# Optimization experiments

Measured on AMD Instinct MI355X. Metric: run time of the kernel, lower is better.

The kernel has to match this reference:

```python
import jax, jax.numpy as jnp
from jax import lax
import numpy as np

B, S, T = 128, 256, 256
VOCAB, EMBED, ENC, DEC, DOF, LOOKBACK = 32000, 256, 256, 512, 4, 4


def setup_inputs() -> dict:
    key = jax.random.key(0)
    ks = jax.random.split(key, 20)
    w = lambda k, shape: jax.random.normal(k, shape, jnp.float32) * 0.05
    return {
        "in_seq": jax.random.randint(ks[0], (B, S), 0, VOCAB),
        "tgt_seq": jax.random.normal(ks[1], (B, T, DOF), jnp.float32),
        "lengths": jnp.full((B,), S, dtype=jnp.int32),
        "embedding": w(ks[2], (VOCAB, EMBED)),
        "enc_Wih_f": w(ks[3], (4 * ENC, EMBED)),
        "enc_Whh_f": w(ks[4], (4 * ENC, ENC)),
        "enc_b_f": w(ks[5], (4 * ENC,)),
        "enc_Wih_b": w(ks[6], (4 * ENC, EMBED)),
        "enc_Whh_b": w(ks[7], (4 * ENC, ENC)),
        "enc_b_b": w(ks[8], (4 * ENC,)),
        "dec_Wih": w(ks[9], (4 * DEC, DEC + LOOKBACK * DOF)),
        "dec_Whh": w(ks[10], (4 * DEC, DEC)),
        "dec_b": w(ks[11], (4 * DEC,)),
        "W_src": w(ks[12], (DEC, 2 * ENC)),
        "W_ctx": w(ks[13], (DEC, 2 * ENC + DEC)),
        "W_out": w(ks[14], (DOF, DEC)),
        "b_out": w(ks[15], (DOF,)),
    }


def _lstm_cell(x, h, c, Wih, Whh, b):
    # PyTorch gate order: i, f, g, o
    g = x @ Wih.T + h @ Whh.T + b
    i, f, gg, o = jnp.split(g, 4, axis=-1)
    c_new = jax.nn.sigmoid(f) * c + jax.nn.sigmoid(i) * jnp.tanh(gg)
    h_new = jax.nn.sigmoid(o) * jnp.tanh(c_new)
    return h_new, c_new


def _scan_lstm(xs, Wih, Whh, b, reverse=False):
    # xs: [T, B, E] -> hidden states [T, B, H] (aligned to original time order)
    Bsz, H = xs.shape[1], Whh.shape[1]
    h0 = jnp.zeros((Bsz, H), xs.dtype)

    def step(carry, x):
        h, c = carry
        h, c = _lstm_cell(x, h, c, Wih, Whh, b)
        return (h, c), h

    _, hs = lax.scan(step, (h0, h0), xs, reverse=reverse)
    return hs


def reference(in_seq, tgt_seq, lengths, embedding,
              enc_Wih_f, enc_Whh_f, enc_b_f,
              enc_Wih_b, enc_Whh_b, enc_b_b,
              dec_Wih, dec_Whh, dec_b,
              W_src, W_ctx, W_out, b_out):
    Bsz, Tlen = tgt_seq.shape[0], tgt_seq.shape[1]
    # ----- encoder (bi-LSTM, eval mode: dropout off, zero initial state) -----
    emb = embedding[in_seq]              # [B,S,E]
    xs = jnp.swapaxes(emb, 0, 1)         # [S,B,E]
    hf = _scan_lstm(xs, enc_Wih_f, enc_Whh_f, enc_b_f, reverse=False)
    hb = _scan_lstm(xs, enc_Wih_b, enc_Whh_b, enc_b_b, reverse=True)
    enc_out = jnp.swapaxes(jnp.concatenate([hf, hb], axis=-1), 0, 1)  # [B,S,2H]
    enc_mask = (in_seq == 0)             # [B,S]
    # precompute attention source projection once (same math as per-step)
    proj = jnp.einsum('bse,de->bsd', enc_out, W_src)  # [B,S,DEC]
    # ----- teacher-forced lookback windows of target frames -----
    pad = jnp.concatenate([jnp.zeros((Bsz, LOOKBACK, DOF), tgt_seq.dtype), tgt_seq], axis=1)
    win = jnp.stack([pad[:, k:k + Tlen] for k in range(LOOKBACK)], axis=2)  # [B,T,LB,DOF]
    win = win.reshape(Bsz, Tlen, LOOKBACK * DOF)
    win_t = jnp.swapaxes(win, 0, 1)      # [T,B,LB*DOF]
    h0 = jnp.zeros((Bsz, DEC), tgt_seq.dtype)

    def step(carry, w_t):
        h, c, feed = carry
        x = jnp.concatenate([w_t, feed], axis=-1)         # [B, LB*DOF + DEC]
        h, c = _lstm_cell(x, h, c, dec_Wih, dec_Whh, dec_b)
        scores = jnp.einsum('bd,bsd->bs', h, proj)        # Luong general score
        scores = jnp.where(enc_mask, -jnp.inf, scores)
        aw = jax.nn.softmax(scores, axis=-1)              # [B,S]
        ctx = jnp.einsum('bs,bse->be', aw, enc_out)       # [B,2H]
        feed = jnp.tanh(jnp.concatenate([h, ctx], axis=-1) @ W_ctx.T)
        out = feed @ W_out.T + b_out                      # [B,DOF]
        return (h, c, feed), (out, aw)

    _, (outs, aws) = lax.scan(step, (h0, h0, h0), win_t)
    dec_outputs = jnp.swapaxes(outs, 0, 1)   # [B,T,DOF]
    attn_weights = jnp.swapaxes(aws, 0, 1)   # [B,T,S]
    outputs = jnp.concatenate(
        [jnp.tanh(dec_outputs[..., :-1]), jax.nn.relu(dec_outputs[..., -1:])], axis=-1)
    return outputs, attn_weights
```

## Files before the change

### kernel.cpp

```cpp
#include <hip/hip_runtime.h>
#include <stdint.h>

#define B 128
#define S 256
#define T 256
#define EMBED 256
#define ENC 256
#define DEC 512
#define DOF 4

typedef __attribute__((ext_vector_type(8))) short bf16x8;
typedef __attribute__((ext_vector_type(4))) float f32x4;

static __device__ __forceinline__ float bf2f(unsigned short u){
  union{uint32_t u;float f;}c; c.u = ((uint32_t)u)<<16; return c.f;
}
static __device__ __forceinline__ unsigned short f2bf(float f){
  union{float f;uint32_t u;}c; c.f=f; uint32_t u=c.u;
  u += 0x7fffu + ((u>>16)&1u);
  return (unsigned short)(u>>16);
}
static __device__ __forceinline__ void unp2(uint32_t w, float&a, float&b){
  union{uint32_t u;float f;}c1,c2; c1.u = w<<16; c2.u = w & 0xffff0000u; a=c1.f; b=c2.f;
}
static __device__ __forceinline__ float sigm(float x){ return 1.0f/(1.0f+__expf(-x)); }

static __device__ __forceinline__ unsigned long long ldc8(const void* p){
  return __hip_atomic_load((unsigned long long*)p, __ATOMIC_RELAXED, __HIP_MEMORY_SCOPE_AGENT);
}
static __device__ __forceinline__ void stc8(void* p, unsigned long long v){
  __hip_atomic_store((unsigned long long*)p, v, __ATOMIC_RELAXED, __HIP_MEMORY_SCOPE_AGENT);
}
static __device__ __forceinline__ void stc4(void* p, unsigned v){
  __hip_atomic_store((unsigned*)p, v, __ATOMIC_RELAXED, __HIP_MEMORY_SCOPE_AGENT);
}
static __device__ __forceinline__ void stc4f(float* p, float v){
  __hip_atomic_store((unsigned*)p, __float_as_uint(v), __ATOMIC_RELAXED, __HIP_MEMORY_SCOPE_AGENT);
}
static __device__ __forceinline__ float ldc4f(const float* p){
  return __uint_as_float(__hip_atomic_load((const unsigned*)p, __ATOMIC_RELAXED, __HIP_MEMORY_SCOPE_AGENT));
}
union F16x8 { unsigned long long q[2]; bf16x8 v; unsigned short s[8]; };
union Ubf   { bf16x8 v; uint32_t u[4]; unsigned short s[8]; };
static __device__ __forceinline__ bf16x8 ldfrag_c(const unsigned short* p){
  F16x8 u; u.q[0] = ldc8(p); u.q[1] = ldc8(p + 4); return u.v;
}
static __device__ __forceinline__ unsigned long long pack4bf(float a,float b,float c,float d){
  return (unsigned long long)f2bf(a) | ((unsigned long long)f2bf(b)<<16)
       | ((unsigned long long)f2bf(c)<<32) | ((unsigned long long)f2bf(d)<<48);
}

#define CLINE 32
#define A_OFF 0
#define F_OFF 128
#define PAIR_OFF 192
#define ENC_OFF 320
static __device__ __forceinline__ unsigned* cl(unsigned* c, int line){ return c + (size_t)line*CLINE; }

static __device__ __forceinline__ void bar_arr(unsigned* line){
  __builtin_amdgcn_s_waitcnt(0);
  __syncthreads();
  if (threadIdx.x == 0)
    __hip_atomic_fetch_add(line, 1u, __ATOMIC_RELAXED, __HIP_MEMORY_SCOPE_AGENT);
}
static __device__ __forceinline__ void barw(unsigned* set, unsigned target, int mask){
  if (threadIdx.x < 64){
    unsigned* p = set + (size_t)(threadIdx.x & mask)*CLINE;
    const int mine = (int)threadIdx.x <= mask;
    for (;;){
      int ok = 1;
      if (mine)
        ok = (int)(__hip_atomic_load(p, __ATOMIC_RELAXED, __HIP_MEMORY_SCOPE_AGENT) >= target);
      if (__all(ok)) break;
      __builtin_amdgcn_s_sleep(8);
    }
  }
  __syncthreads();
  asm volatile("" ::: "memory");
}

static __device__ __forceinline__ int enc_idx(int s, int c){
  return s*256 + (((c & 24) | ((c ^ s) & 7)) << 3);
}

__global__ __launch_bounds__(256,1) void k_encoder(
  const unsigned short* __restrict__ emb,
  const unsigned short* __restrict__ WF, const unsigned short* __restrict__ WB,
  const float* __restrict__ bF, const float* __restrict__ bB,
  unsigned short* __restrict__ hEnc,
  unsigned short* __restrict__ encOut,
  unsigned* __restrict__ cntBase)
{
  __shared__ __align__(16) unsigned short Ws[16*520];
  __shared__ __align__(16) float Gs[64*17];
  __shared__ float bsh[16];
  const int bid = blockIdx.x;
  const int dir = bid >> 7;
  const int mg  = (bid >> 6) & 1;
  const int ng  = bid & 63;
  const int tid = threadIdx.x;
  const int lane = tid & 63, w = tid >> 6;
  const int l16 = lane & 15, qd = lane >> 4;
  const int m_base = mg * 64;
  unsigned* mycnt = cntBase + (size_t)dir*16*CLINE;
  unsigned* myline = cl(mycnt, bid & 15);

  const unsigned short* Wg = (dir ? WB : WF) + (size_t)ng*16*512;
  for (int i = tid; i < 16*64; i += 256){
    const int r = i >> 6, s = i & 63;
    *(uint4*)&Ws[r*520 + s*8] = *(const uint4*)&Wg[r*512 + s*8];
  }
  if (tid < 16) bsh[tid] = (dir ? bB : bF)[ng*16 + tid];
  float c[4] = {0.f,0.f,0.f,0.f};
  __syncthreads();

  for (int t = 0; t < S; ++t){
    const int tt = dir ? (S-1-t) : t;
    const unsigned short* Ae = emb + ((size_t)tt*B + m_base + w*16 + l16)*256 + qd*8;
    bf16x8 av[8];
#pragma unroll
    for (int ks = 0; ks < 8; ++ks) av[ks] = *(const bf16x8*)(Ae + ks*32);
    if (t) barw(mycnt, (unsigned)(8u*(unsigned)t), 15);
    const unsigned short* Ah = hEnc + (((size_t)dir*2 + (size_t)(t&1))*B + m_base + w*16 + l16)*256 + qd*8;
    bf16x8 hf[8];
#pragma unroll
    for (int ks = 0; ks < 8; ++ks) hf[ks] = ldfrag_c(Ah + ks*32);
    f32x4 acc = (f32x4){0.f,0.f,0.f,0.f};
#pragma unroll
    for (int ks = 0; ks < 8; ++ks){
      bf16x8 bb = *(const bf16x8*)&Ws[l16*520 + ks*32 + qd*8];
      acc = __builtin_amdgcn_mfma_f32_16x16x32_bf16(av[ks], bb, acc, 0, 0, 0);
    }
#pragma unroll
    for (int ks = 0; ks < 8; ++ks){
      bf16x8 bb = *(const bf16x8*)&Ws[l16*520 + 256 + ks*32 + qd*8];
      acc = __builtin_amdgcn_mfma_f32_16x16x32_bf16(hf[ks], bb, acc, 0, 0, 0);
    }
    __syncthreads();
#pragma unroll
    for (int r = 0; r < 4; ++r)
      Gs[(w*16 + qd*4 + r)*17 + l16] = acc[r];
    __syncthreads();
    if (tid < 64){
      const int bl = tid;
      float hv[4];
#pragma unroll
      for (int u = 0; u < 4; ++u){
        const float gi = Gs[bl*17 + u*4 + 0] + bsh[u*4 + 0];
        const float gf = Gs[bl*17 + u*4 + 1] + bsh[u*4 + 1];
        const float gg = Gs[bl*17 + u*4 + 2] + bsh[u*4 + 2];
        const float go = Gs[bl*17 + u*4 + 3] + bsh[u*4 + 3];
        const float cn = sigm(gf)*c[u] + sigm(gi)*tanhf(gg);
        c[u] = cn;
        hv[u] = sigm(go)*tanhf(cn);
      }
      const int b2 = m_base + bl;
      const unsigned long long hq = pack4bf(hv[0],hv[1],hv[2],hv[3]);
      stc8(&hEnc[(((size_t)dir*2 + (size_t)((t+1)&1))*B + b2)*256 + ng*4], hq);
      *(unsigned long long*)&encOut[((size_t)b2*S + tt)*512 + dir*256 + ng*4] = hq;
    }
    bar_arr(myline);
  }
}

__global__ __launch_bounds__(256,2) void k_proj(
  const unsigned short* __restrict__ encOut,
  const unsigned short* __restrict__ WSP,
  const unsigned short* __restrict__ WCP,
  unsigned short* __restrict__ proj,
  unsigned short* __restrict__ encW)
{
  const int nb = blockIdx.x & 7;
  const int mt = blockIdx.x >> 3;
  const int tid = threadIdx.x;
  const int lane = tid & 63, w = tid >> 6;
  const int l16 = lane & 15, qd = lane >> 4;
  const int m0 = mt*64 + w*16;
  const unsigned short* Ap = encOut + ((size_t)m0 + l16)*512 + qd*8;
  bf16x8 av[16];
#pragma unroll
  for (int ks = 0; ks < 16; ++ks) av[ks] = *(const bf16x8*)(Ap + ks*32);
  for (int which = 0; which < 2; ++which){
    const unsigned short* Wb = which ? WCP : WSP;
    unsigned short* outp = which ? encW : proj;
    for (int nn = 0; nn < 4; ++nn){
      const int qn = nb*4 + nn;
      const unsigned short* Bq = Wb + (size_t)qn*16*512 + (size_t)lane*8;
      f32x4 acc = (f32x4){0.f,0.f,0.f,0.f};
#pragma unroll
      for (int ks = 0; ks < 16; ++ks){
        bf16x8 bb = *(const bf16x8*)(Bq + (size_t)ks*512);
        acc = __builtin_amdgcn_mfma_f32_16x16x32_bf16(av[ks], bb, acc, 0, 0, 0);
      }
      const int d = qn*16 + l16, dh = d >> 8, dl = d & 255;
#pragma unroll
      for (int r = 0; r < 4; ++r){
        const int m = m0 + qd*4 + r;
        const int bb2 = m >> 8, s = m & 255;
        outp[(((size_t)bb2*2 + dh)*256 + s)*256 + dl] = f2bf(acc[r]);
      }
    }
  }
}

__global__ __launch_bounds__(256,1) void k_decoder(
  const unsigned short* __restrict__ win,
  const unsigned short* __restrict__ WDx,
  const float* __restrict__ bD,
  const unsigned short* __restrict__ WhP,
  const unsigned short* __restrict__ projq,
  const unsigned short* __restrict__ encWq,
  const int* __restrict__ in_seq,
  const float* __restrict__ Wout, const float* __restrict__ bout,
  unsigned short* __restrict__ hdec,
  unsigned short* __restrict__ feed,
  float* __restrict__ scp,
  float* __restrict__ out_main, float* __restrict__ out_attn,
  unsigned* __restrict__ cnts)
{
  __shared__ __align__(16) unsigned short encS[65536];
  __shared__ __align__(16) float scrf[2080];
  __shared__ float bsh[16];
  const int bid = blockIdx.x;
  const int b  = bid >> 1, eh = bid & 1;
  const int mg = bid & 1, ng = (bid >> 1) & 127;
  const int tid = threadIdx.x;
  const int lane = tid & 63, w = tid >> 6;
  const int l16 = lane & 15, qd = lane >> 4;
  const int m_base = mg*64;

  if (tid < 16) bsh[tid] = bD[ng*16 + tid];
  const int mymask = (in_seq[b*S + tid] == 0);
  {
    const unsigned short* Pq = projq + (((size_t)b*2 + eh)*256)*256;
    for (int i = 0; i < 32; ++i){
      const int s = i*8 + (tid>>5), cc = tid & 31;
      const uint4 v = *(const uint4*)&Pq[(size_t)s*256 + cc*8];
      *(uint4*)&encS[enc_idx(s, cc)] = v;
    }
  }
  bf16x8 ev[32];
  {
    const int cc = lane & 31, par = lane >> 5;
    const unsigned short* Ep = encWq + (((size_t)b*2 + eh)*256)*256 + cc*8;
#pragma unroll
    for (int i2 = 0; i2 < 32; ++i2)
      ev[i2] = *(const bf16x8*)(Ep + (size_t)(w*64 + i2*2 + par)*256);
  }
  float c[4] = {0.f,0.f,0.f,0.f};
  __syncthreads();

  for (int t = 0; t < T; ++t){
    const int row = m_base + w*16 + l16;
    const unsigned short* Aw = win  + ((size_t)t*B + row)*64 + qd*8;
    const unsigned short* Af = feed + (size_t)row*512 + qd*8;
    const unsigned short* Ah = hdec + ((size_t)(t&1)*B + row)*512 + qd*8;
    const unsigned short* Bp = WDx + (size_t)ng*34*512 + (size_t)lane*8;
    f32x4 acc = (f32x4){0.f,0.f,0.f,0.f};
#pragma unroll
    for (int ch = 0; ch < 2; ++ch){
      bf16x8 hv[8];
#pragma unroll
      for (int i = 0; i < 8; ++i) hv[i] = ldfrag_c(Ah + (ch*8 + i)*32);
#pragma unroll
      for (int ks = 0; ks < 8; ++ks){
        bf16x8 bb = *(const bf16x8*)(Bp + (size_t)(18 + ch*8 + ks)*512);
        acc = __builtin_amdgcn_mfma_f32_16x16x32_bf16(hv[ks], bb, acc, 0, 0, 0);
      }
    }
    bf16x8 a0 = *(const bf16x8*)(Aw);
    bf16x8 a1 = *(const bf16x8*)(Aw + 32);
    if (t){
      if (bid & 1) barw(cl(cnts, F_OFF), (unsigned)(4u*(unsigned)t), 63);
      else         barw(cl(cnts, F_OFF), (unsigned)(4u*(unsigned)t), 31);
    }
    {
      bf16x8 b0 = *(const bf16x8*)(Bp);
      bf16x8 b1 = *(const bf16x8*)(Bp + 512);
      acc = __builtin_amdgcn_mfma_f32_16x16x32_bf16(a0, b0, acc, 0, 0, 0);
      acc = __builtin_amdgcn_mfma_f32_16x16x32_bf16(a1, b1, acc, 0, 0, 0);
    }
#pragma unroll
    for (int ch = 0; ch < 2; ++ch){
      bf16x8 av[8], bv[8];
#pragma unroll
      for (int i = 0; i < 8; ++i){
        av[i] = ldfrag_c(Af + (ch*8 + i)*32);
        bv[i] = *(const bf16x8*)(Bp + (size_t)(2 + ch*8 + i)*512);
      }
#pragma unroll
      for (int ks = 0; ks < 8; ++ks)
        acc = __builtin_amdgcn_mfma_f32_16x16x32_bf16(av[ks], bv[ks], acc, 0, 0, 0);
    }
    __syncthreads();
#pragma unroll
    for (int r = 0; r < 4; ++r)
      scrf[(w*16 + qd*4 + r)*17 + l16] = acc[r];
    __syncthreads();
    if (tid < 64){
      float hv[4];
#pragma unroll
      for (int u = 0; u < 4; ++u){
        const float gi = scrf[tid*17 + u*4 + 0] + bsh[u*4 + 0];
        const float gf = scrf[tid*17 + u*4 + 1] + bsh[u*4 + 1];
        const float gg = scrf[tid*17 + u*4 + 2] + bsh[u*4 + 2];
        const float go = scrf[tid*17 + u*4 + 3] + bsh[u*4 + 3];
        const float cn = sigm(gf)*c[u] + sigm(gi)*tanhf(gg);
        c[u] = cn;
        hv[u] = sigm(go)*tanhf(cn);
      }
      stc8(&hdec[((size_t)((t+1)&1)*B + m_base + tid)*512 + ng*4],
           pack4bf(hv[0],hv[1],hv[2],hv[3]));
    }
    bar_arr(cl(cnts, A_OFF + (bid & 63)));

    if ((bid & 1) && t > 0){
      const int b2o = bid >> 1;
      const int d = tid >> 6, kk = lane;
      const unsigned short* fp = feed + (size_t)b2o*512 + kk*8;
      F16x8 u; u.q[0] = ldc8(fp); u.q[1] = ldc8(fp + 4);
      const float* wp = Wout + d*512 + kk*8;
      float p = 0.f;
#pragma unroll
      for (int j2 = 0; j2 < 8; ++j2) p += bf2f(u.s[j2]) * wp[j2];
#pragma unroll
      for (int off = 32; off > 0; off >>= 1) p += __shfl_down(p, off, 64);
      if (kk == 0){
        const float v = p + bout[d];
        out_main[((size_t)b2o*T + (t-1))*4 + d] = (d < 3) ? tanhf(v) : fmaxf(v, 0.f);
      }
    }

    barw(cl(cnts, A_OFF), (unsigned)(4u*(unsigned)(t+1)), 63);
    if (tid < 64){
      const unsigned short* hp = hdec + ((size_t)((t+1)&1)*B + b)*512 + tid*8;
      F16x8 uh; uh.q[0] = ldc8(hp); uh.q[1] = ldc8(hp + 4);
#pragma unroll
      for (int j = 0; j < 8; ++j) scrf[tid*8 + j] = bf2f(uh.s[j]);
    }
    __syncthreads();
    float sc = 0.f;
#pragma unroll 8
    for (int cix = 0; cix < 32; ++cix){
      Ubf u8; u8.v = *(const bf16x8*)&encS[enc_idx(tid, cix)];
      float f0,f1,f2,f3,f4,f5,f6,f7;
      unp2(u8.u[0],f0,f1); unp2(u8.u[1],f2,f3); unp2(u8.u[2],f4,f5); unp2(u8.u[3],f6,f7);
      const float* qp = &scrf[eh*256 + cix*8];
      sc += f0*qp[0] + f1*qp[1] + f2*qp[2] + f3*qp[3]
          + f4*qp[4] + f5*qp[5] + f6*qp[6] + f7*qp[7];
    }
    stc4f(&scp[((size_t)b*2 + eh)*256 + tid], sc);
    __builtin_amdgcn_s_waitcnt(0);
    __syncthreads();
    if (tid == 0)
      __hip_atomic_fetch_add(cl(cnts, PAIR_OFF + b), 1u, __ATOMIC_RELAXED, __HIP_MEMORY_SCOPE_AGENT);
    float hw0 = 0.f, hw1 = 0.f, hw2 = 0.f, hw3 = 0.f;
    {
      const unsigned short* Wp = WhP + (size_t)(eh*256 + tid)*8;
#pragma unroll 8
      for (int kc = 0; kc < 64; ++kc){
        Ubf u8; u8.v = *(const bf16x8*)(Wp + (size_t)kc*4096);
        const float4 h0 = *(const float4*)&scrf[kc*8];
        const float4 h1 = *(const float4*)&scrf[kc*8 + 4];
        float f0,f1,f2,f3,f4,f5,f6,f7;
        unp2(u8.u[0],f0,f1); unp2(u8.u[1],f2,f3); unp2(u8.u[2],f4,f5); unp2(u8.u[3],f6,f7);
        hw0 += h0.x*f0 + h1.x*f4;
        hw1 += h0.y*f1 + h1.y*f5;
        hw2 += h0.z*f2 + h1.z*f6;
        hw3 += h0.w*f3 + h1.w*f7;
      }
    }
    const float hw = (hw0 + hw1) + (hw2 + hw3);
    if (tid == 0){
      unsigned* pp = cl(cnts, PAIR_OFF + b);
      while (__hip_atomic_load(pp, __ATOMIC_RELAXED, __HIP_MEMORY_SCOPE_AGENT) < 2u*(unsigned)(t+1))
        __builtin_amdgcn_s_sleep(4);
    }
    __syncthreads();
    asm volatile("" ::: "memory");
    float tot = sc + ldc4f(&scp[((size_t)b*2 + (1-eh))*256 + tid]);
    if (mymask) tot = -1e30f;
    float mx = tot;
#pragma unroll
    for (int off = 32; off > 0; off >>= 1) mx = fmaxf(mx, __shfl_xor(mx, off, 64));
    if (lane == 0) scrf[768 + w] = mx;
    __syncthreads();
    mx = fmaxf(fmaxf(scrf[768], scrf[769]), fmaxf(scrf[770], scrf[771]));
    const float e = __expf(tot - mx);
    float l = e;
#pragma unroll
    for (int off = 32; off > 0; off >>= 1) l += __shfl_xor(l, off, 64);
    if (lane == 0) scrf[772 + w] = l;
    __syncthreads();
    l = scrf[772] + scrf[773] + scrf[774] + scrf[775];
    const float aw = e / l;
    scrf[512 + tid] = aw;
    if (eh == 0) __builtin_nontemporal_store(aw, &out_attn[((size_t)b*T + t)*S + tid]);
    __syncthreads();
    {
      float a[8] = {0,0,0,0,0,0,0,0};
      const int cc = lane & 31, par = lane >> 5;
#pragma unroll
      for (int i2 = 0; i2 < 32; ++i2){
        const int srow = w*64 + i2*2 + par;
        const float wgt = scrf[512 + srow];
        Ubf u8; u8.v = ev[i2];
        float f0,f1,f2,f3,f4,f5,f6,f7;
        unp2(u8.u[0],f0,f1); unp2(u8.u[1],f2,f3); unp2(u8.u[2],f4,f5); unp2(u8.u[3],f6,f7);
        a[0]+=wgt*f0; a[1]+=wgt*f1; a[2]+=wgt*f2; a[3]+=wgt*f3;
        a[4]+=wgt*f4; a[5]+=wgt*f5; a[6]+=wgt*f6; a[7]+=wgt*f7;
      }
#pragma unroll
      for (int j2 = 0; j2 < 8; ++j2) a[j2] += __shfl_xor(a[j2], 32, 64);
      if (par == 0){
#pragma unroll
        for (int j2 = 0; j2 < 8; ++j2) scrf[784 + w*256 + cc*8 + j2] = a[j2];
      }
    }
    __syncthreads();
    {
      const float v = scrf[784 + tid] + scrf[784 + 256 + tid]
                    + scrf[784 + 512 + tid] + scrf[784 + 768 + tid];
      scrf[1808 + tid] = tanhf(hw + v);
    }
    __syncthreads();
    if (tid < 128){
      const int n2 = tid*2;
      stc4(&feed[(size_t)b*512 + eh*256 + n2],
           (unsigned)f2bf(scrf[1808 + n2]) | ((unsigned)f2bf(scrf[1808 + n2 + 1]) << 16));
    }
    bar_arr(cl(cnts, F_OFF + (bid >> 2)));
  }
  if (bid & 1){
    barw(cl(cnts, F_OFF), (unsigned)(4u*256u), 63);
    const int b2o = bid >> 1;
    const int d = tid >> 6, kk = lane;
    const unsigned short* fp = feed + (size_t)b2o*512 + kk*8;
    F16x8 u; u.q[0] = ldc8(fp); u.q[1] = ldc8(fp + 4);
    const float* wp = Wout + d*512 + kk*8;
    float p = 0.f;
#pragma unroll
    for (int j2 = 0; j2 < 8; ++j2) p += bf2f(u.s[j2]) * wp[j2];
#pragma unroll
    for (int off = 32; off > 0; off >>= 1) p += __shfl_down(p, off, 64);
    if (kk == 0){
      const float v = p + bout[d];
      out_main[((size_t)b2o*T + 255)*4 + d] = (d < 3) ? tanhf(v) : fmaxf(v, 0.f);
    }
  }
}

__global__ __launch_bounds__(256) void k_build_encw(
  const float* __restrict__ WihF, const float* __restrict__ WhhF,
  const float* __restrict__ WihB, const float* __restrict__ WhhB,
  unsigned short* WF, unsigned short* WB)
{
  const int idx = blockIdx.x*256 + threadIdx.x;
  const int dir = idx >> 19;
  const int i2 = idx & 524287;
  const int row = i2 >> 9, col = i2 & 511;
  const int j = row >> 2, g = row & 3;
  const int orig = g*256 + j;
  const float* Wih = dir ? WihB : WihF;
  const float* Whh = dir ? WhhB : WhhF;
  const float v = (col < 256) ? Wih[orig*256 + col] : Whh[orig*256 + (col-256)];
  (dir ? WB : WF)[i2] = f2bf(v);
}

__global__ __launch_bounds__(256) void k_build_decw(
  const float* __restrict__ Wih, const float* __restrict__ Whh, unsigned short* WDx)
{
  const int idx = blockIdx.x*256 + threadIdx.x;
  if (idx >= 2048*1088) return;
  const int row = idx / 1088, col = idx - row*1088;
  const int j = row >> 2, g = row & 3;
  const int orig = g*512 + j;
  float v;
  if (col < 16)        v = Wih[orig*528 + col];
  else if (col < 64)   v = 0.f;
  else if (col < 576)  v = Wih[orig*528 + (col - 48)];
  else                 v = Whh[orig*512 + (col - 576)];
  const int ng = row >> 4, l16 = row & 15;
  const int ks = col >> 5, qdd = (col >> 3) & 3, jj = col & 7;
  WDx[(((size_t)ng*34 + ks)*64 + qdd*16 + l16)*8 + jj] = f2bf(v);
}

__global__ __launch_bounds__(256) void k_build_whp(
  const float* __restrict__ Wctx, unsigned short* WhP)
{
  const int idx = blockIdx.x*256 + threadIdx.x;
  const int k = idx >> 9, n = idx & 511;
  WhP[(((size_t)(k >> 3)*512 + n) << 3) + (k & 7)] = f2bf(Wctx[(size_t)n*1024 + k]);
}

__global__ __launch_bounds__(256) void k_build_wcp(
  const float* __restrict__ Wctx, unsigned short* WCP)
{
  const int idx = blockIdx.x*256 + threadIdx.x;
  const int n = idx >> 9, e = idx & 511;
  const int qn = n >> 4, l16 = n & 15;
  const int ks = e >> 5, qdd = (e >> 3) & 3, jj = e & 7;
  WCP[(((size_t)qn*16 + ks)*64 + qdd*16 + l16)*8 + jj] = f2bf(Wctx[(size_t)n*1024 + 512 + e]);
}

__global__ __launch_bounds__(256) void k_build_wsp(
  const float* __restrict__ Wsrc, unsigned short* WSP)
{
  const int idx = blockIdx.x*256 + threadIdx.x;
  const int d = idx >> 9, e = idx & 511;
  const int qn = d >> 4, l16 = d & 15;
  const int ks = e >> 5, qdd = (e >> 3) & 3, jj = e & 7;
  WSP[(((size_t)qn*16 + ks)*64 + qdd*16 + l16)*8 + jj] = f2bf(Wsrc[(size_t)d*512 + e]);
}

__global__ __launch_bounds__(256) void k_build_bias(
  const float* __restrict__ ebF, const float* __restrict__ ebB,
  const float* __restrict__ dB, float* bF, float* bB, float* bD)
{
  const int idx = blockIdx.x*256 + threadIdx.x;
  if (idx < 1024) bF[idx] = ebF[(idx&3)*256 + (idx>>2)];
  else if (idx < 2048){ const int i = idx-1024; bB[i] = ebB[(i&3)*256 + (i>>2)]; }
  else { const int i = idx-2048; bD[i] = dB[(i&3)*512 + (i>>2)]; }
}

__global__ __launch_bounds__(256) void k_embed(
  const int* __restrict__ in_seq, const float* __restrict__ table, unsigned short* emb)
{
  const int idx = blockIdx.x*256 + threadIdx.x;
  const int e = idx & 255, b = (idx >> 8) & 127, s = idx >> 15;
  const int tok = in_seq[b*S + s];
  emb[idx] = f2bf(table[(size_t)tok*256 + e]);
}

__global__ __launch_bounds__(256) void k_win(
  const float* __restrict__ tgt, unsigned short* win)
{
  const int idx = blockIdx.x*256 + threadIdx.x;
  const int c = idx & 63, b = (idx >> 6) & 127, t = idx >> 13;
  float v = 0.f;
  if (c < 16){
    const int k = c >> 2, jj = c & 3;
    const int ts = t + k - 4;
    if (ts >= 0) v = tgt[((size_t)b*T + ts)*4 + jj];
  }
  win[idx] = f2bf(v);
}

extern "C" void kernel_launch(void* const* d_in, const int* in_sizes, int n_in,
                              void* d_out, int out_size, void* d_ws, size_t ws_size,
                              hipStream_t stream)
{
  const int*   in_seq    = (const int*)d_in[0];
  const float* tgt       = (const float*)d_in[1];
  const float* embedding = (const float*)d_in[3];
  const float* eWihF = (const float*)d_in[4];
  const float* eWhhF = (const float*)d_in[5];
  const float* ebF   = (const float*)d_in[6];
  const float* eWihB = (const float*)d_in[7];
  const float* eWhhB = (const float*)d_in[8];
  const float* ebB   = (const float*)d_in[9];
  const float* dWih  = (const float*)d_in[10];
  const float* dWhh  = (const float*)d_in[11];
  const float* dB    = (const float*)d_in[12];
  const float* Wsrc  = (const float*)d_in[13];
  const float* Wctx  = (const float*)d_in[14];
  const float* Wout  = (const float*)d_in[15];
  const float* bout  = (const float*)d_in[16];

  char* ws = (char*)d_ws;
  size_t off = 0;
  auto al = [&](size_t bytes)->char*{
    char* p = ws + off; off += (bytes + 255) & ~(size_t)255; return p; };

  char* stateBase = ws;
  unsigned short* hEnc = (unsigned short*)al(262144);
  unsigned short* hdec = (unsigned short*)al(262144);
  unsigned short* feed = (unsigned short*)al(131072);
  unsigned*       cnts = (unsigned*)al(45056);
  const size_t stateBytes = off;

  unsigned short* emb    = (unsigned short*)al(16777216);
  unsigned short* win    = (unsigned short*)al(4194304);
  unsigned short* encOut = (unsigned short*)al(33554432);
  unsigned short* proj   = (unsigned short*)al(33554432);
  unsigned short* encWq  = (unsigned short*)al(33554432);
  unsigned short* WF     = (unsigned short*)al(1048576);
  unsigned short* WB     = (unsigned short*)al(1048576);
  unsigned short* WDx    = (unsigned short*)al(4456448);
  unsigned short* WhP    = (unsigned short*)al(524288);
  unsigned short* WCP    = (unsigned short*)al(524288);
  unsigned short* WSP    = (unsigned short*)al(524288);
  float*          scp    = (float*)al(262144);
  float* bFr = (float*)al(4096);
  float* bBr = (float*)al(4096);
  float* bDr = (float*)al(8192);
  (void)ws_size; (void)in_sizes; (void)n_in; (void)out_size;

  float* out_main = (float*)d_out;
  float* out_attn = out_main + (size_t)B*T*DOF;

  const dim3 blk(256);
  k_build_encw <<<4096,  blk, 0, stream>>>(eWihF, eWhhF, eWihB, eWhhB, WF, WB);
  k_build_decw <<<8704,  blk, 0, stream>>>(dWih, dWhh, WDx);
  k_build_whp  <<<1024,  blk, 0, stream>>>(Wctx, WhP);
  k_build_wcp  <<<1024,  blk, 0, stream>>>(Wctx, WCP);
  k_build_wsp  <<<1024,  blk, 0, stream>>>(Wsrc, WSP);
  k_build_bias <<<16,    blk, 0, stream>>>(ebF, ebB, dB, bFr, bBr, bDr);
  k_embed      <<<32768, blk, 0, stream>>>(in_seq, embedding, emb);
  k_win        <<<8192,  blk, 0, stream>>>(tgt, win);
  hipMemsetAsync(stateBase, 0, stateBytes, stream);

  k_encoder<<<256, blk, 0, stream>>>(emb, WF, WB, bFr, bBr, hEnc, encOut,
                                     cnts + (size_t)ENC_OFF*CLINE);

  k_proj<<<4096, blk, 0, stream>>>(encOut, WSP, WCP, proj, encWq);

  k_decoder<<<256, blk, 0, stream>>>(win, WDx, bDr, WhP, proj, encWq, in_seq,
                                     Wout, bout, hdec, feed, scp,
                                     out_main, out_attn, cnts);
}
```

Before: 8.789 ms.

## Partition decoder gate GEMM by batch group to localize cross-block barriers

The decoder's per-step gate GEMM is re-partitioned so each group of 32 blocks owns 16 batch rows and all 2048 gate columns, instead of splitting by 64-row halves and 16-column slices. The grid-wide hdec and feed barriers shrink to per-group barriers over 32 counters, and the attention phase only waits on blocks in its own batch group. This cuts global synchronisation fan-in and lets groups run independently. In exchange, each block now reads all decoder weight columns for its slice and the counter area doubles in size.

```diff
diff --git a/kernel.cpp b/kernel.cpp
--- a/kernel.cpp
+++ b/kernel.cpp
@@ -52,9 +52,9 @@
 
 #define CLINE 32
 #define A_OFF 0
-#define F_OFF 128
-#define PAIR_OFF 192
-#define ENC_OFF 320
+#define F_OFF 256
+#define PAIR_OFF 512
+#define ENC_OFF 640
 static __device__ __forceinline__ unsigned* cl(unsigned* c, int line){ return c + (size_t)line*CLINE; }
 
 static __device__ __forceinline__ void bar_arr(unsigned* line){
@@ -220,16 +220,18 @@
 {
   __shared__ __align__(16) unsigned short encS[65536];
   __shared__ __align__(16) float scrf[2080];
-  __shared__ float bsh[16];
+  __shared__ float bsh[64];
   const int bid = blockIdx.x;
-  const int b  = bid >> 1, eh = bid & 1;
-  const int mg = bid & 1, ng = (bid >> 1) & 127;
+  const int j = bid & 31, g = bid >> 5;
+  const int gb0 = g*16;
+  const int b  = gb0 + (j >> 1), eh = j & 1;
   const int tid = threadIdx.x;
   const int lane = tid & 63, w = tid >> 6;
   const int l16 = lane & 15, qd = lane >> 4;
-  const int m_base = mg*64;
-
-  if (tid < 16) bsh[tid] = bD[ng*16 + tid];
+  unsigned* Aset = cl(cnts, A_OFF + g*32);
+  unsigned* Fset = cl(cnts, F_OFF + g*32);
+
+  if (tid < 64) bsh[tid] = bD[j*64 + tid];
   const int mymask = (in_seq[b*S + tid] == 0);
   {
     const unsigned short* Pq = projq + (((size_t)b*2 + eh)*256)*256;
@@ -247,15 +249,14 @@
     for (int i2 = 0; i2 < 32; ++i2)
       ev[i2] = *(const bf16x8*)(Ep + (size_t)(w*64 + i2*2 + par)*256);
   }
-  float c[4] = {0.f,0.f,0.f,0.f};
+  float cst = 0.f;
   __syncthreads();
 
   for (int t = 0; t < T; ++t){
-    const int row = m_base + w*16 + l16;
-    const unsigned short* Aw = win  + ((size_t)t*B + row)*64 + qd*8;
-    const unsigned short* Af = feed + (size_t)row*512 + qd*8;
-    const unsigned short* Ah = hdec + ((size_t)(t&1)*B + row)*512 + qd*8;
-    const unsigned short* Bp = WDx + (size_t)ng*34*512 + (size_t)lane*8;
+    const unsigned short* Aw = win  + ((size_t)t*B + gb0 + l16)*64 + qd*8;
+    const unsigned short* Af = feed + (size_t)(gb0 + l16)*512 + qd*8;
+    const unsigned short* Ah = hdec + ((size_t)(t&1)*B + gb0 + l16)*512 + qd*8;
+    const unsigned short* Bp = WDx + (size_t)(j*4 + w)*34*512 + (size_t)lane*8;
     f32x4 acc = (f32x4){0.f,0.f,0.f,0.f};
 #pragma unroll
     for (int ch = 0; ch < 2; ++ch){
@@ -270,10 +271,7 @@
     }
     bf16x8 a0 = *(const bf16x8*)(Aw);
     bf16x8 a1 = *(const bf16x8*)(Aw + 32);
-    if (t){
-      if (bid & 1) barw(cl(cnts, F_OFF), (unsigned)(4u*(unsigned)t), 63);
-      else         barw(cl(cnts, F_OFF), (unsigned)(4u*(unsigned)t), 31);
-    }
+    if (t) barw(Fset, (unsigned)t, 31);
     {
       bf16x8 b0 = *(const bf16x8*)(Bp);
       bf16x8 b1 = *(const bf16x8*)(Bp + 512);
@@ -295,29 +293,30 @@
     __syncthreads();
 #pragma unroll
     for (int r = 0; r < 4; ++r)
-      scrf[(w*16 + qd*4 + r)*17 + l16] = acc[r];
-    __syncthreads();
-    if (tid < 64){
-      float hv[4];
-#pragma unroll
-      for (int u = 0; u < 4; ++u){
-        const float gi = scrf[tid*17 + u*4 + 0] + bsh[u*4 + 0];
-        const float gf = scrf[tid*17 + u*4 + 1] + bsh[u*4 + 1];
-        const float gg = scrf[tid*17 + u*4 + 2] + bsh[u*4 + 2];
-        const float go = scrf[tid*17 + u*4 + 3] + bsh[u*4 + 3];
-        const float cn = sigm(gf)*c[u] + sigm(gi)*tanhf(gg);
-        c[u] = cn;
-        hv[u] = sigm(go)*tanhf(cn);
-      }
-      stc8(&hdec[((size_t)((t+1)&1)*B + m_base + tid)*512 + ng*4],
-           pack4bf(hv[0],hv[1],hv[2],hv[3]));
-    }
-    bar_arr(cl(cnts, A_OFF + (bid & 63)));
-
-    if ((bid & 1) && t > 0){
-      const int b2o = bid >> 1;
+      scrf[(qd*4 + r)*68 + w*17 + l16] = acc[r];
+    __syncthreads();
+    {
+      const int bl = tid >> 4, di = tid & 15;
+      const int ws = di >> 2, u = di & 3;
+      const float gi = scrf[bl*68 + ws*17 + u*4 + 0] + bsh[ws*16 + u*4 + 0];
+      const float gf = scrf[bl*68 + ws*17 + u*4 + 1] + bsh[ws*16 + u*4 + 1];
+      const float gg = scrf[bl*68 + ws*17 + u*4 + 2] + bsh[ws*16 + u*4 + 2];
+      const float go = scrf[bl*68 + ws*17 + u*4 + 3] + bsh[ws*16 + u*4 + 3];
+      const float cn = sigm(gf)*cst + sigm(gi)*tanhf(gg);
+      cst = cn;
+      const float hv = sigm(go)*tanhf(cn);
+      const float v1 = __shfl_down(hv, 1, 64);
+      const float v2 = __shfl_down(hv, 2, 64);
+      const float v3 = __shfl_down(hv, 3, 64);
+      if ((di & 3) == 0)
+        stc8(&hdec[((size_t)((t+1)&1)*B + gb0 + bl)*512 + j*16 + di],
+             pack4bf(hv, v1, v2, v3));
+    }
+    bar_arr(cl(cnts, A_OFF + bid));
+
+    if ((j & 1) && t > 0){
       const int d = tid >> 6, kk = lane;
-      const unsigned short* fp = feed + (size_t)b2o*512 + kk*8;
+      const unsigned short* fp = feed + (size_t)b*512 + kk*8;
       F16x8 u; u.q[0] = ldc8(fp); u.q[1] = ldc8(fp + 4);
       const float* wp = Wout + d*512 + kk*8;
       float p = 0.f;
@@ -327,16 +326,16 @@
       for (int off = 32; off > 0; off >>= 1) p += __shfl_down(p, off, 64);
       if (kk == 0){
         const float v = p + bout[d];
-        out_main[((size_t)b2o*T + (t-1))*4 + d] = (d < 3) ? tanhf(v) : fmaxf(v, 0.f);
-      }
-    }
-
-    barw(cl(cnts, A_OFF), (unsigned)(4u*(unsigned)(t+1)), 63);
+        out_main[((size_t)b*T + (t-1))*4 + d] = (d < 3) ? tanhf(v) : fmaxf(v, 0.f);
+      }
+    }
+
+    barw(Aset, (unsigned)(t+1), 31);
     if (tid < 64){
       const unsigned short* hp = hdec + ((size_t)((t+1)&1)*B + b)*512 + tid*8;
       F16x8 uh; uh.q[0] = ldc8(hp); uh.q[1] = ldc8(hp + 4);
 #pragma unroll
-      for (int j = 0; j < 8; ++j) scrf[tid*8 + j] = bf2f(uh.s[j]);
+      for (int jj = 0; jj < 8; ++jj) scrf[tid*8 + jj] = bf2f(uh.s[jj]);
     }
     __syncthreads();
     float sc = 0.f;
@@ -429,13 +428,12 @@
       stc4(&feed[(size_t)b*512 + eh*256 + n2],
            (unsigned)f2bf(scrf[1808 + n2]) | ((unsigned)f2bf(scrf[1808 + n2 + 1]) << 16));
     }
-    bar_arr(cl(cnts, F_OFF + (bid >> 2)));
-  }
-  if (bid & 1){
-    barw(cl(cnts, F_OFF), (unsigned)(4u*256u), 63);
-    const int b2o = bid >> 1;
+    bar_arr(cl(cnts, F_OFF + bid));
+  }
+  if (j & 1){
+    barw(Fset, 256u, 31);
     const int d = tid >> 6, kk = lane;
-    const unsigned short* fp = feed + (size_t)b2o*512 + kk*8;
+    const unsigned short* fp = feed + (size_t)b*512 + kk*8;
     F16x8 u; u.q[0] = ldc8(fp); u.q[1] = ldc8(fp + 4);
     const float* wp = Wout + d*512 + kk*8;
     float p = 0.f;
@@ -445,7 +443,7 @@
     for (int off = 32; off > 0; off >>= 1) p += __shfl_down(p, off, 64);
     if (kk == 0){
       const float v = p + bout[d];
-      out_main[((size_t)b2o*T + 255)*4 + d] = (d < 3) ? tanhf(v) : fmaxf(v, 0.f);
+      out_main[((size_t)b*T + 255)*4 + d] = (d < 3) ? tanhf(v) : fmaxf(v, 0.f);
     }
   }
 }
@@ -576,7 +574,7 @@
   unsigned short* hEnc = (unsigned short*)al(262144);
   unsigned short* hdec = (unsigned short*)al(262144);
   unsigned short* feed = (unsigned short*)al(131072);
-  unsigned*       cnts = (unsigned*)al(45056);
+  unsigned*       cnts = (unsigned*)al(90112);
   const size_t stateBytes = off;
 
   unsigned short* emb    = (unsigned short*)al(16777216);
```

New measurement: 8.594 ms. 2.2% less time.
